# Kernel optimization log

Measured on AMD Instinct MI355X. Metric: run time of the kernel, lower is better.

## Reference

```python
import jax, jax.numpy as jnp
import numpy as np

P, N, C_IN, C_OUT = 40000, 32, 4, 64
C_AUG = C_IN + 5  # +3 cluster offsets, +2 center offsets -> 9
VX, VY = 0.2, 0.2
X_OFF = VX / 2 + 0.0      # 0.1
Y_OFF = VY / 2 + (-40.0)  # -39.9
BN_EPS = 1e-3


def setup_inputs() -> dict:
    key = jax.random.key(0)
    k1, k2, k3, k4, k5, k6, k7 = jax.random.split(key, 7)
    features = jax.random.normal(k1, (P, N, C_IN), dtype=jnp.float32)
    # at least 1 real point per pillar
    num_voxels = jax.random.randint(k2, (P,), 1, N + 1, dtype=jnp.int32)
    cx = jax.random.randint(k3, (P,), 0, 352, dtype=jnp.int32)  # x grid index (coors[:,3])
    cy = jax.random.randint(k4, (P,), 0, 400, dtype=jnp.int32)  # y grid index (coors[:,2])
    zeros = jnp.zeros((P,), dtype=jnp.int32)
    coors = jnp.stack([zeros, zeros, cy, cx], axis=1)  # [P,4] = (batch, z, y, x)
    linear_w = jax.random.normal(k5, (C_OUT, C_AUG), dtype=jnp.float32) * 0.1  # torch Linear weight [out,in], bias=False
    gamma = 1.0 + 0.1 * jax.random.normal(k6, (C_OUT,), dtype=jnp.float32)
    beta = 0.1 * jax.random.normal(k7, (C_OUT,), dtype=jnp.float32)
    return {
        "features": features,
        "num_voxels": num_voxels,
        "coors": coors,
        "linear_w": linear_w,
        "gamma": gamma,
        "beta": beta,
        "batch_size": 4,
    }


def reference(features, num_voxels, coors, linear_w, gamma, beta, batch_size):
    # batch_size=4 and P > 2500 -> lidar branch (self.linear / self.norm) of PFNLayer.
    dtype = features.dtype
    nv = num_voxels.astype(dtype)[:, None, None]  # [P,1,1]
    xyz = features[:, :, :3]
    points_mean = jnp.sum(xyz, axis=1, keepdims=True) / nv            # [P,1,3]
    f_cluster = xyz - points_mean                                     # [P,N,3]
    fcx = features[:, :, 0] - (coors[:, 3].astype(dtype)[:, None] * VX + X_OFF)
    fcy = features[:, :, 1] - (coors[:, 2].astype(dtype)[:, None] * VY + Y_OFF)
    f_center = jnp.stack([fcx, fcy], axis=-1)                         # [P,N,2]
    feats = jnp.concatenate([features, f_cluster, f_center], axis=-1)  # [P,N,9]
    # zero out padded points
    mask = (jnp.arange(N)[None, :] < num_voxels[:, None]).astype(dtype)[:, :, None]
    feats = feats * mask
    # Linear (no bias): [P,N,9] x [64,9]^T -> [P,N,64]
    x = jnp.einsum('pnc,uc->pnu', feats, linear_w)
    # BatchNorm1d in training mode: stats over (pillars, points) per channel, eps=1e-3
    mean = jnp.mean(x, axis=(0, 1))
    var = jnp.var(x, axis=(0, 1))
    x = (x - mean) * jax.lax.rsqrt(var + BN_EPS) * gamma + beta
    x = jax.nn.relu(x)
    # max over points, last_layer -> no concat; squeeze -> [P,64]
    return jnp.max(x, axis=1)
```

## Files before the change

kernel.cpp:

```cpp
#include <hip/hip_runtime.h>
#include <hip/hip_fp16.h>
#include <float.h>
#include <math.h>

#define PPIL   40000
#define NPTS   32
#define COUT   64
#define PPB    16
#define NBLK_F 2500
#define PSTRIDE 132
#define NSB_F  16
#define NFB    625

__device__ __forceinline__ float shfl_xor_f(float v, int m) {
    return __shfl_xor(v, m, 64);
}

__device__ __forceinline__ void weight_prep(const float* __restrict__ linear_w,
                                            float* lds_w, int tid)
{
    if (tid < 64) {
        const float* wr = linear_w + tid * 9;
        const float w0 = wr[0], w1 = wr[1], w2 = wr[2], w3 = wr[3], w4 = wr[4];
        const float w5 = wr[5], w6 = wr[6], w7 = wr[7], w8 = wr[8];
        float* dw = &lds_w[tid * 9];
        dw[0] = w0 + w4 + w7;
        dw[1] = w1 + w5 + w8;
        dw[2] = w2 + w6;
        dw[3] = w3;
        dw[4] = w4; dw[5] = w5; dw[6] = w6; dw[7] = w7; dw[8] = w8;
    }
}

__global__ __launch_bounds__(128) void pfn_main(
    const float* __restrict__ features, const int* __restrict__ num_voxels,
    const int* __restrict__ coors, const float* __restrict__ linear_w,
    __half* __restrict__ rawh, float* __restrict__ partials)
{
    __shared__ float lds_f[PPB * PSTRIDE];
    __shared__ float lds_w[64 * 9];

    const int tid = threadIdx.x;
    const int bid = blockIdx.x;
    const int pl2 = tid >> 3;
    const int cg  = tid & 7;
    const int p   = bid * PPB + pl2;

    weight_prep(linear_w, lds_w, tid);

    const int   nvi = num_voxels[p];
    const float nvf = (float)nvi;
    const float axp = (float)coors[p * 4 + 3] * 0.2f + 0.1f;
    const float byp = (float)coors[p * 4 + 2] * 0.2f - 39.9f;

    float sx = 0.f, sy = 0.f, sz = 0.f;
    float t0 = 0.f, t1 = 0.f, t2 = 0.f, t3 = 0.f;
    #pragma unroll
    for (int i = 0; i < 4; ++i) {
        const int n = cg + 8 * i;
        const float4 f = *(const float4*)(features + ((size_t)p * NPTS + n) * 4);
        *(float4*)&lds_f[pl2 * PSTRIDE + n * 4] = f;
        sx += f.x; sy += f.y; sz += f.z;
        const float m = (n < nvi) ? 1.0f : 0.0f;
        t0 = fmaf(f.x, m, t0); t1 = fmaf(f.y, m, t1);
        t2 = fmaf(f.z, m, t2); t3 = fmaf(f.w, m, t3);
    }
    #pragma unroll
    for (int m = 1; m <= 4; m <<= 1) {
        sx += shfl_xor_f(sx, m); sy += shfl_xor_f(sy, m); sz += shfl_xor_f(sz, m);
        t0 += shfl_xor_f(t0, m); t1 += shfl_xor_f(t1, m);
        t2 += shfl_xor_f(t2, m); t3 += shfl_xor_f(t3, m);
    }
    const float inv = 1.0f / nvf;
    const float mxp = sx * inv, myp = sy * inv, mzp = sz * inv;

    __syncthreads();

    float g0[8], g1[8], g2[8], g3[8], cc[8];
    #pragma unroll
    for (int k = 0; k < 8; ++k) {
        const float* wp = &lds_w[(cg * 8 + k) * 9];
        g0[k] = wp[0]; g1[k] = wp[1]; g2[k] = wp[2]; g3[k] = wp[3];
        cc[k] = -(wp[4] * mxp + wp[5] * myp + wp[6] * mzp + wp[7] * axp + wp[8] * byp);
    }

    float s2v[8], mxv[8];
    #pragma unroll
    for (int k = 0; k < 8; ++k) { s2v[k] = 0.0f; mxv[k] = -FLT_MAX; }

    const float4* fb = (const float4*)&lds_f[pl2 * PSTRIDE];
    for (int n = 0; n < nvi; ++n) {
        const float4 f = fb[n];
        #pragma unroll
        for (int k = 0; k < 8; ++k) {
            float x = fmaf(g0[k], f.x, cc[k]);
            x = fmaf(g1[k], f.y, x);
            x = fmaf(g2[k], f.z, x);
            x = fmaf(g3[k], f.w, x);
            s2v[k] = fmaf(x, x, s2v[k]);
            mxv[k] = fmaxf(mxv[k], x);
        }
    }
    if (nvi < NPTS) {
        #pragma unroll
        for (int k = 0; k < 8; ++k) mxv[k] = fmaxf(mxv[k], 0.0f);
    }

    float s1v[8];
    #pragma unroll
    for (int k = 0; k < 8; ++k) {
        float d = g0[k] * t0;
        d = fmaf(g1[k], t1, d);
        d = fmaf(g2[k], t2, d);
        d = fmaf(g3[k], t3, d);
        s1v[k] = fmaf(nvf, cc[k], d);
    }

    {
        __half2 h0 = __floats2half2_rn(mxv[0], mxv[1]);
        __half2 h1 = __floats2half2_rn(mxv[2], mxv[3]);
        __half2 h2 = __floats2half2_rn(mxv[4], mxv[5]);
        __half2 h3 = __floats2half2_rn(mxv[6], mxv[7]);
        uint4 pk;
        pk.x = *(const unsigned int*)&h0;
        pk.y = *(const unsigned int*)&h1;
        pk.z = *(const unsigned int*)&h2;
        pk.w = *(const unsigned int*)&h3;
        *(uint4*)(rawh + (size_t)p * COUT + cg * 8) = pk;
    }

    __syncthreads();
    float* lsum = lds_f;
    *(float4*)&lsum[pl2 * 128 + cg * 8 + 0]      = make_float4(s1v[0], s1v[1], s1v[2], s1v[3]);
    *(float4*)&lsum[pl2 * 128 + cg * 8 + 4]      = make_float4(s1v[4], s1v[5], s1v[6], s1v[7]);
    *(float4*)&lsum[pl2 * 128 + 64 + cg * 8 + 0] = make_float4(s2v[0], s2v[1], s2v[2], s2v[3]);
    *(float4*)&lsum[pl2 * 128 + 64 + cg * 8 + 4] = make_float4(s2v[4], s2v[5], s2v[6], s2v[7]);
    __syncthreads();

    float acc = 0.0f;
    #pragma unroll
    for (int r = 0; r < 16; ++r) acc += lsum[r * 128 + tid];
    partials[bid * 128 + tid] = acc;
}

__global__ __launch_bounds__(1024) void pfn_stats16(
    const float* __restrict__ partials, float* __restrict__ partials2)
{
    __shared__ double red[32][128];
    const int t = threadIdx.x, b = blockIdx.x;
    const int col4 = t & 31, j = t >> 5;
    const float4* p4 = (const float4*)partials;

    double a0 = 0.0, a1 = 0.0, a2 = 0.0, a3 = 0.0;
    #pragma unroll
    for (int i = 0; i < 5; ++i) {
        const int r = b + NSB_F * (j + 32 * i);
        if (r < NBLK_F) {
            const float4 v = p4[r * 32 + col4];
            a0 += (double)v.x; a1 += (double)v.y;
            a2 += (double)v.z; a3 += (double)v.w;
        }
    }
    red[j][col4 * 4 + 0] = a0;
    red[j][col4 * 4 + 1] = a1;
    red[j][col4 * 4 + 2] = a2;
    red[j][col4 * 4 + 3] = a3;
    __syncthreads();
    if (t < 128) {
        double s = 0.0;
        #pragma unroll
        for (int jj = 0; jj < 32; ++jj) s += red[jj][t];
        partials2[b * 128 + t] = (float)s;
    }
}

__global__ __launch_bounds__(1024) void pfn_final(
    const float* __restrict__ partials2, const float* __restrict__ gamma,
    const float* __restrict__ beta, const __half* __restrict__ rawh,
    float* __restrict__ out)
{
    __shared__ double red[128];
    __shared__ float  sb[128];
    const int t = threadIdx.x;
    if (t < 128) {
        double s = 0.0;
        #pragma unroll
        for (int b = 0; b < NSB_F; ++b) s += (double)partials2[b * 128 + t];
        red[t] = s;
    }
    __syncthreads();
    if (t < 64) {
        const float s1 = (float)red[t];
        const float s2 = (float)red[64 + t];
        const float invPN = 1.0f / ((float)PPIL * (float)NPTS);
        const float mean  = s1 * invPN;
        const float var   = fmaf(-mean, mean, s2 * invPN);
        const float scale = gamma[t] * rsqrtf(var + 1e-3f);
        sb[t]      = scale;
        sb[64 + t] = fmaf(-mean, scale, beta[t]);
    }
    __syncthreads();

    const int i  = blockIdx.x * 1024 + t;
    const int u0 = (i & 15) * 4;
    const uint2 pk = *(const uint2*)(rawh + (size_t)i * 4);
    const __half2 h01 = *(const __half2*)&pk.x;
    const __half2 h23 = *(const __half2*)&pk.y;
    float4 v;
    v.x = fmaxf(fmaf(__low2float(h01),  sb[u0 + 0], sb[64 + u0 + 0]), 0.0f);
    v.y = fmaxf(fmaf(__high2float(h01), sb[u0 + 1], sb[64 + u0 + 1]), 0.0f);
    v.z = fmaxf(fmaf(__low2float(h23),  sb[u0 + 2], sb[64 + u0 + 2]), 0.0f);
    v.w = fmaxf(fmaf(__high2float(h23), sb[u0 + 3], sb[64 + u0 + 3]), 0.0f);
    ((float4*)out)[i] = v;
}

extern "C" void kernel_launch(void* const* d_in, const int* in_sizes, int n_in,
                              void* d_out, int out_size, void* d_ws, size_t ws_size,
                              hipStream_t stream) {
    const float* features   = (const float*)d_in[0];
    const int*   num_voxels = (const int*)d_in[1];
    const int*   coors      = (const int*)d_in[2];
    const float* linear_w   = (const float*)d_in[3];
    const float* gamma      = (const float*)d_in[4];
    const float* beta       = (const float*)d_in[5];

    float*  out       = (float*)d_out;
    float*  wsf       = (float*)d_ws;
    float*  partials  = wsf;
    float*  partials2 = wsf + NBLK_F * 128;
    __half* rawh      = (__half*)(wsf + (1 << 20));

    pfn_main<<<NBLK_F, 128, 0, stream>>>(features, num_voxels, coors,
                                         linear_w, rawh, partials);
    pfn_stats16<<<NSB_F, 1024, 0, stream>>>(partials, partials2);
    pfn_final<<<NFB, 1024, 0, stream>>>(partials2, gamma, beta, rawh, out);
}
```

Baseline: 30.53 us.

## Process two pillar groups per block with register-prefetched second group

Each main-kernel block now handles 32 pillars in two sequential halves. The second half's features are loaded into registers while the first half computes. The weight-load and stats-reduction overhead is shared across both halves, and the partial-sum count and the stats kernel loop bounds are halved. The intent is to hide global-load latency and cut per-block fixed costs. The cost is fewer blocks (1250), higher register pressure from the prefetched float4s and the kept w4..w8 arrays, and possibly lower occupancy.

```diff
diff --git a/kernel.cpp b/kernel.cpp
--- a/kernel.cpp
+++ b/kernel.cpp
@@ -7,7 +7,7 @@
 #define NPTS   32
 #define COUT   64
 #define PPB    16
-#define NBLK_F 2500
+#define NBLK_M 1250
 #define PSTRIDE 132
 #define NSB_F  16
 #define NFB    625
@@ -32,6 +32,18 @@
     }
 }
 
+__device__ __forceinline__ void pillar_butterfly(
+    float& sx, float& sy, float& sz,
+    float& t0, float& t1, float& t2, float& t3)
+{
+    #pragma unroll
+    for (int m = 1; m <= 4; m <<= 1) {
+        sx += shfl_xor_f(sx, m); sy += shfl_xor_f(sy, m); sz += shfl_xor_f(sz, m);
+        t0 += shfl_xor_f(t0, m); t1 += shfl_xor_f(t1, m);
+        t2 += shfl_xor_f(t2, m); t3 += shfl_xor_f(t3, m);
+    }
+}
+
 __global__ __launch_bounds__(128) void pfn_main(
     const float* __restrict__ features, const int* __restrict__ num_voxels,
     const int* __restrict__ coors, const float* __restrict__ linear_w,
@@ -44,79 +56,85 @@
     const int bid = blockIdx.x;
     const int pl2 = tid >> 3;
     const int cg  = tid & 7;
-    const int p   = bid * PPB + pl2;
+    const int pA  = bid * (2 * PPB) + pl2;
+    const int pB  = bid * (2 * PPB) + PPB + pl2;
 
     weight_prep(linear_w, lds_w, tid);
 
-    const int   nvi = num_voxels[p];
-    const float nvf = (float)nvi;
-    const float axp = (float)coors[p * 4 + 3] * 0.2f + 0.1f;
-    const float byp = (float)coors[p * 4 + 2] * 0.2f - 39.9f;
-
-    float sx = 0.f, sy = 0.f, sz = 0.f;
-    float t0 = 0.f, t1 = 0.f, t2 = 0.f, t3 = 0.f;
+    const int   nviA = num_voxels[pA];
+    const float nvfA = (float)nviA;
+    const float axA  = (float)coors[pA * 4 + 3] * 0.2f + 0.1f;
+    const float byA  = (float)coors[pA * 4 + 2] * 0.2f - 39.9f;
+
+    float sxA = 0.f, syA = 0.f, szA = 0.f;
+    float tA0 = 0.f, tA1 = 0.f, tA2 = 0.f, tA3 = 0.f;
     #pragma unroll
     for (int i = 0; i < 4; ++i) {
         const int n = cg + 8 * i;
-        const float4 f = *(const float4*)(features + ((size_t)p * NPTS + n) * 4);
+        const float4 f = *(const float4*)(features + ((size_t)pA * NPTS + n) * 4);
         *(float4*)&lds_f[pl2 * PSTRIDE + n * 4] = f;
-        sx += f.x; sy += f.y; sz += f.z;
-        const float m = (n < nvi) ? 1.0f : 0.0f;
-        t0 = fmaf(f.x, m, t0); t1 = fmaf(f.y, m, t1);
-        t2 = fmaf(f.z, m, t2); t3 = fmaf(f.w, m, t3);
-    }
-    #pragma unroll
-    for (int m = 1; m <= 4; m <<= 1) {
-        sx += shfl_xor_f(sx, m); sy += shfl_xor_f(sy, m); sz += shfl_xor_f(sz, m);
-        t0 += shfl_xor_f(t0, m); t1 += shfl_xor_f(t1, m);
-        t2 += shfl_xor_f(t2, m); t3 += shfl_xor_f(t3, m);
-    }
-    const float inv = 1.0f / nvf;
-    const float mxp = sx * inv, myp = sy * inv, mzp = sz * inv;
-
-    __syncthreads();
-
-    float g0[8], g1[8], g2[8], g3[8], cc[8];
+        sxA += f.x; syA += f.y; szA += f.z;
+        const float m = (n < nviA) ? 1.0f : 0.0f;
+        tA0 = fmaf(f.x, m, tA0); tA1 = fmaf(f.y, m, tA1);
+        tA2 = fmaf(f.z, m, tA2); tA3 = fmaf(f.w, m, tA3);
+    }
+    pillar_butterfly(sxA, syA, szA, tA0, tA1, tA2, tA3);
+    const float invA = 1.0f / nvfA;
+    const float mxpA = sxA * invA, mypA = syA * invA, mzpA = szA * invA;
+
+    __syncthreads();
+
+    const int   nviB = num_voxels[pB];
+    const float nvfB = (float)nviB;
+    const float axB  = (float)coors[pB * 4 + 3] * 0.2f + 0.1f;
+    const float byB  = (float)coors[pB * 4 + 2] * 0.2f - 39.9f;
+    float4 fB[4];
+    #pragma unroll
+    for (int i = 0; i < 4; ++i) {
+        const int n = cg + 8 * i;
+        fB[i] = *(const float4*)(features + ((size_t)pB * NPTS + n) * 4);
+    }
+
+    float g0[8], g1[8], g2[8], g3[8], w4[8], w5[8], w6[8], w7[8], w8[8];
+    float cc[8];
     #pragma unroll
     for (int k = 0; k < 8; ++k) {
         const float* wp = &lds_w[(cg * 8 + k) * 9];
         g0[k] = wp[0]; g1[k] = wp[1]; g2[k] = wp[2]; g3[k] = wp[3];
-        cc[k] = -(wp[4] * mxp + wp[5] * myp + wp[6] * mzp + wp[7] * axp + wp[8] * byp);
-    }
-
-    float s2v[8], mxv[8];
-    #pragma unroll
-    for (int k = 0; k < 8; ++k) { s2v[k] = 0.0f; mxv[k] = -FLT_MAX; }
-
-    const float4* fb = (const float4*)&lds_f[pl2 * PSTRIDE];
-    for (int n = 0; n < nvi; ++n) {
-        const float4 f = fb[n];
+        w4[k] = wp[4]; w5[k] = wp[5]; w6[k] = wp[6]; w7[k] = wp[7]; w8[k] = wp[8];
+        cc[k] = -(w4[k] * mxpA + w5[k] * mypA + w6[k] * mzpA + w7[k] * axA + w8[k] * byA);
+    }
+
+    float s1acc[8], s2acc[8], mxv[8];
+
+    #pragma unroll
+    for (int k = 0; k < 8; ++k) { s2acc[k] = 0.0f; mxv[k] = -FLT_MAX; }
+    {
+        const float4* fb = (const float4*)&lds_f[pl2 * PSTRIDE];
+        for (int n = 0; n < nviA; ++n) {
+            const float4 f = fb[n];
+            #pragma unroll
+            for (int k = 0; k < 8; ++k) {
+                float x = fmaf(g0[k], f.x, cc[k]);
+                x = fmaf(g1[k], f.y, x);
+                x = fmaf(g2[k], f.z, x);
+                x = fmaf(g3[k], f.w, x);
+                s2acc[k] = fmaf(x, x, s2acc[k]);
+                mxv[k]   = fmaxf(mxv[k], x);
+            }
+        }
+        if (nviA < NPTS) {
+            #pragma unroll
+            for (int k = 0; k < 8; ++k) mxv[k] = fmaxf(mxv[k], 0.0f);
+        }
         #pragma unroll
         for (int k = 0; k < 8; ++k) {
-            float x = fmaf(g0[k], f.x, cc[k]);
-            x = fmaf(g1[k], f.y, x);
-            x = fmaf(g2[k], f.z, x);
-            x = fmaf(g3[k], f.w, x);
-            s2v[k] = fmaf(x, x, s2v[k]);
-            mxv[k] = fmaxf(mxv[k], x);
-        }
-    }
-    if (nvi < NPTS) {
-        #pragma unroll
-        for (int k = 0; k < 8; ++k) mxv[k] = fmaxf(mxv[k], 0.0f);
-    }
-
-    float s1v[8];
-    #pragma unroll
-    for (int k = 0; k < 8; ++k) {
-        float d = g0[k] * t0;
-        d = fmaf(g1[k], t1, d);
-        d = fmaf(g2[k], t2, d);
-        d = fmaf(g3[k], t3, d);
-        s1v[k] = fmaf(nvf, cc[k], d);
-    }
-
-    {
+            float d = g0[k] * tA0;
+            d = fmaf(g1[k], tA1, d);
+            d = fmaf(g2[k], tA2, d);
+            d = fmaf(g3[k], tA3, d);
+            s1acc[k] = fmaf(nvfA, cc[k], d);
+        }
         __half2 h0 = __floats2half2_rn(mxv[0], mxv[1]);
         __half2 h1 = __floats2half2_rn(mxv[2], mxv[3]);
         __half2 h2 = __floats2half2_rn(mxv[4], mxv[5]);
@@ -126,15 +144,78 @@
         pk.y = *(const unsigned int*)&h1;
         pk.z = *(const unsigned int*)&h2;
         pk.w = *(const unsigned int*)&h3;
-        *(uint4*)(rawh + (size_t)p * COUT + cg * 8) = pk;
+        *(uint4*)(rawh + (size_t)pA * COUT + cg * 8) = pk;
+    }
+
+    __syncthreads();
+
+    float sxB = 0.f, syB = 0.f, szB = 0.f;
+    float tB0 = 0.f, tB1 = 0.f, tB2 = 0.f, tB3 = 0.f;
+    #pragma unroll
+    for (int i = 0; i < 4; ++i) {
+        const int n = cg + 8 * i;
+        *(float4*)&lds_f[pl2 * PSTRIDE + n * 4] = fB[i];
+        sxB += fB[i].x; syB += fB[i].y; szB += fB[i].z;
+        const float m = (n < nviB) ? 1.0f : 0.0f;
+        tB0 = fmaf(fB[i].x, m, tB0); tB1 = fmaf(fB[i].y, m, tB1);
+        tB2 = fmaf(fB[i].z, m, tB2); tB3 = fmaf(fB[i].w, m, tB3);
+    }
+    pillar_butterfly(sxB, syB, szB, tB0, tB1, tB2, tB3);
+    const float invB = 1.0f / nvfB;
+    const float mxpB = sxB * invB, mypB = syB * invB, mzpB = szB * invB;
+    #pragma unroll
+    for (int k = 0; k < 8; ++k)
+        cc[k] = -(w4[k] * mxpB + w5[k] * mypB + w6[k] * mzpB + w7[k] * axB + w8[k] * byB);
+    __syncthreads();
+
+    {
+        float s2v[8];
+        #pragma unroll
+        for (int k = 0; k < 8; ++k) { s2v[k] = 0.0f; mxv[k] = -FLT_MAX; }
+        const float4* fb = (const float4*)&lds_f[pl2 * PSTRIDE];
+        for (int n = 0; n < nviB; ++n) {
+            const float4 f = fb[n];
+            #pragma unroll
+            for (int k = 0; k < 8; ++k) {
+                float x = fmaf(g0[k], f.x, cc[k]);
+                x = fmaf(g1[k], f.y, x);
+                x = fmaf(g2[k], f.z, x);
+                x = fmaf(g3[k], f.w, x);
+                s2v[k] = fmaf(x, x, s2v[k]);
+                mxv[k] = fmaxf(mxv[k], x);
+            }
+        }
+        if (nviB < NPTS) {
+            #pragma unroll
+            for (int k = 0; k < 8; ++k) mxv[k] = fmaxf(mxv[k], 0.0f);
+        }
+        #pragma unroll
+        for (int k = 0; k < 8; ++k) {
+            float d = g0[k] * tB0;
+            d = fmaf(g1[k], tB1, d);
+            d = fmaf(g2[k], tB2, d);
+            d = fmaf(g3[k], tB3, d);
+            s1acc[k] += fmaf(nvfB, cc[k], d);
+            s2acc[k] += s2v[k];
+        }
+        __half2 h0 = __floats2half2_rn(mxv[0], mxv[1]);
+        __half2 h1 = __floats2half2_rn(mxv[2], mxv[3]);
+        __half2 h2 = __floats2half2_rn(mxv[4], mxv[5]);
+        __half2 h3 = __floats2half2_rn(mxv[6], mxv[7]);
+        uint4 pk;
+        pk.x = *(const unsigned int*)&h0;
+        pk.y = *(const unsigned int*)&h1;
+        pk.z = *(const unsigned int*)&h2;
+        pk.w = *(const unsigned int*)&h3;
+        *(uint4*)(rawh + (size_t)pB * COUT + cg * 8) = pk;
     }
 
     __syncthreads();
     float* lsum = lds_f;
-    *(float4*)&lsum[pl2 * 128 + cg * 8 + 0]      = make_float4(s1v[0], s1v[1], s1v[2], s1v[3]);
-    *(float4*)&lsum[pl2 * 128 + cg * 8 + 4]      = make_float4(s1v[4], s1v[5], s1v[6], s1v[7]);
-    *(float4*)&lsum[pl2 * 128 + 64 + cg * 8 + 0] = make_float4(s2v[0], s2v[1], s2v[2], s2v[3]);
-    *(float4*)&lsum[pl2 * 128 + 64 + cg * 8 + 4] = make_float4(s2v[4], s2v[5], s2v[6], s2v[7]);
+    *(float4*)&lsum[pl2 * 128 + cg * 8 + 0]      = make_float4(s1acc[0], s1acc[1], s1acc[2], s1acc[3]);
+    *(float4*)&lsum[pl2 * 128 + cg * 8 + 4]      = make_float4(s1acc[4], s1acc[5], s1acc[6], s1acc[7]);
+    *(float4*)&lsum[pl2 * 128 + 64 + cg * 8 + 0] = make_float4(s2acc[0], s2acc[1], s2acc[2], s2acc[3]);
+    *(float4*)&lsum[pl2 * 128 + 64 + cg * 8 + 4] = make_float4(s2acc[4], s2acc[5], s2acc[6], s2acc[7]);
     __syncthreads();
 
     float acc = 0.0f;
@@ -153,9 +234,9 @@
 
     double a0 = 0.0, a1 = 0.0, a2 = 0.0, a3 = 0.0;
     #pragma unroll
-    for (int i = 0; i < 5; ++i) {
+    for (int i = 0; i < 3; ++i) {
         const int r = b + NSB_F * (j + 32 * i);
-        if (r < NBLK_F) {
+        if (r < NBLK_M) {
             const float4 v = p4[r * 32 + col4];
             a0 += (double)v.x; a1 += (double)v.y;
             a2 += (double)v.z; a3 += (double)v.w;
@@ -227,10 +308,10 @@
     float*  out       = (float*)d_out;
     float*  wsf       = (float*)d_ws;
     float*  partials  = wsf;
-    float*  partials2 = wsf + NBLK_F * 128;
+    float*  partials2 = wsf + NBLK_M * 128;
     __half* rawh      = (__half*)(wsf + (1 << 20));
 
-    pfn_main<<<NBLK_F, 128, 0, stream>>>(features, num_voxels, coors,
+    pfn_main<<<NBLK_M, 128, 0, stream>>>(features, num_voxels, coors,
                                          linear_w, rawh, partials);
     pfn_stats16<<<NSB_F, 1024, 0, stream>>>(partials, partials2);
     pfn_final<<<NFB, 1024, 0, stream>>>(partials2, gamma, beta, rawh, out);
```

After: 31.90 us. 4.5% more time.

## Remap main kernel so each lane owns one output channel across pillars

Applied to the files above, without the earlier changes.

The main kernel now uses 256-thread blocks covering 32 pillars. Instead of 8 threads per pillar each handling 8 channels, each wave lane owns one channel and loops over 8 pillars, reading per-pillar constants staged in LDS. The point loop is unrolled by two. This is meant to cut register pressure and block count and to balance work across variable nv, at the cost of 2-byte scattered half stores instead of 16-byte packed stores and a serial loop over pillars per wave.

```diff
diff --git a/kernel.cpp b/kernel.cpp
--- a/kernel.cpp
+++ b/kernel.cpp
@@ -6,8 +6,8 @@
 #define PPIL   40000
 #define NPTS   32
 #define COUT   64
-#define PPB    16
-#define NBLK_F 2500
+#define PPB    32
+#define NBLK_M 1250
 #define PSTRIDE 132
 #define NSB_F  16
 #define NFB    625
@@ -16,9 +16,20 @@
     return __shfl_xor(v, m, 64);
 }
 
-__device__ __forceinline__ void weight_prep(const float* __restrict__ linear_w,
-                                            float* lds_w, int tid)
+__global__ __launch_bounds__(256) void pfn_main(
+    const float* __restrict__ features, const int* __restrict__ num_voxels,
+    const int* __restrict__ coors, const float* __restrict__ linear_w,
+    __half* __restrict__ rawh, float* __restrict__ partials)
 {
+    __shared__ float lds_f[PPB * PSTRIDE];
+    __shared__ float lds_pc[PPB][12];
+    __shared__ float lds_w[64 * 9];
+    __shared__ float lds_red[4][128];
+
+    const int tid = threadIdx.x;
+    const int bid = blockIdx.x;
+    const int pb  = bid * PPB;
+
     if (tid < 64) {
         const float* wr = linear_w + tid * 9;
         const float w0 = wr[0], w1 = wr[1], w2 = wr[2], w3 = wr[3], w4 = wr[4];
@@ -30,117 +41,111 @@
         dw[3] = w3;
         dw[4] = w4; dw[5] = w5; dw[6] = w6; dw[7] = w7; dw[8] = w8;
     }
-}
-
-__global__ __launch_bounds__(128) void pfn_main(
-    const float* __restrict__ features, const int* __restrict__ num_voxels,
-    const int* __restrict__ coors, const float* __restrict__ linear_w,
-    __half* __restrict__ rawh, float* __restrict__ partials)
-{
-    __shared__ float lds_f[PPB * PSTRIDE];
-    __shared__ float lds_w[64 * 9];
-
-    const int tid = threadIdx.x;
-    const int bid = blockIdx.x;
-    const int pl2 = tid >> 3;
-    const int cg  = tid & 7;
-    const int p   = bid * PPB + pl2;
-
-    weight_prep(linear_w, lds_w, tid);
-
-    const int   nvi = num_voxels[p];
-    const float nvf = (float)nvi;
-    const float axp = (float)coors[p * 4 + 3] * 0.2f + 0.1f;
-    const float byp = (float)coors[p * 4 + 2] * 0.2f - 39.9f;
-
-    float sx = 0.f, sy = 0.f, sz = 0.f;
-    float t0 = 0.f, t1 = 0.f, t2 = 0.f, t3 = 0.f;
+
+    {
+        const int pl  = tid >> 3, sub = tid & 7;
+        const int p   = pb + pl;
+        const int nvi = num_voxels[p];
+        float sx = 0.f, sy = 0.f, sz = 0.f;
+        float t0 = 0.f, t1 = 0.f, t2 = 0.f, t3 = 0.f;
+        #pragma unroll
+        for (int i = 0; i < 4; ++i) {
+            const int n = sub + 8 * i;
+            const float4 f = *(const float4*)(features + ((size_t)p * NPTS + n) * 4);
+            *(float4*)&lds_f[pl * PSTRIDE + n * 4] = f;
+            sx += f.x; sy += f.y; sz += f.z;
+            const float m = (n < nvi) ? 1.0f : 0.0f;
+            t0 = fmaf(f.x, m, t0); t1 = fmaf(f.y, m, t1);
+            t2 = fmaf(f.z, m, t2); t3 = fmaf(f.w, m, t3);
+        }
+        #pragma unroll
+        for (int m = 1; m <= 4; m <<= 1) {
+            sx += shfl_xor_f(sx, m); sy += shfl_xor_f(sy, m); sz += shfl_xor_f(sz, m);
+            t0 += shfl_xor_f(t0, m); t1 += shfl_xor_f(t1, m);
+            t2 += shfl_xor_f(t2, m); t3 += shfl_xor_f(t3, m);
+        }
+        if (sub == 0) {
+            const float nvf = (float)nvi;
+            const float inv = 1.0f / nvf;
+            float* pc = lds_pc[pl];
+            pc[0] = sx * inv;
+            pc[1] = sy * inv;
+            pc[2] = sz * inv;
+            pc[3] = (float)coors[p * 4 + 3] * 0.2f + 0.1f;
+            pc[4] = (float)coors[p * 4 + 2] * 0.2f - 39.9f;
+            pc[5] = nvf;
+            pc[6] = t0; pc[7] = t1; pc[8] = t2; pc[9] = t3;
+        }
+    }
+    __syncthreads();
+
+    const int w    = tid >> 6;
+    const int lane = tid & 63;
+
+    const float* wp = &lds_w[lane * 9];
+    const float g0 = wp[0], g1 = wp[1], g2 = wp[2], g3 = wp[3];
+    const float w4 = wp[4], w5 = wp[5], w6 = wp[6], w7 = wp[7], w8 = wp[8];
+
+    float s1acc = 0.0f, s2acc = 0.0f;
+
     #pragma unroll
-    for (int i = 0; i < 4; ++i) {
-        const int n = cg + 8 * i;
-        const float4 f = *(const float4*)(features + ((size_t)p * NPTS + n) * 4);
-        *(float4*)&lds_f[pl2 * PSTRIDE + n * 4] = f;
-        sx += f.x; sy += f.y; sz += f.z;
-        const float m = (n < nvi) ? 1.0f : 0.0f;
-        t0 = fmaf(f.x, m, t0); t1 = fmaf(f.y, m, t1);
-        t2 = fmaf(f.z, m, t2); t3 = fmaf(f.w, m, t3);
-    }
-    #pragma unroll
-    for (int m = 1; m <= 4; m <<= 1) {
-        sx += shfl_xor_f(sx, m); sy += shfl_xor_f(sy, m); sz += shfl_xor_f(sz, m);
-        t0 += shfl_xor_f(t0, m); t1 += shfl_xor_f(t1, m);
-        t2 += shfl_xor_f(t2, m); t3 += shfl_xor_f(t3, m);
-    }
-    const float inv = 1.0f / nvf;
-    const float mxp = sx * inv, myp = sy * inv, mzp = sz * inv;
-
-    __syncthreads();
-
-    float g0[8], g1[8], g2[8], g3[8], cc[8];
-    #pragma unroll
-    for (int k = 0; k < 8; ++k) {
-        const float* wp = &lds_w[(cg * 8 + k) * 9];
-        g0[k] = wp[0]; g1[k] = wp[1]; g2[k] = wp[2]; g3[k] = wp[3];
-        cc[k] = -(wp[4] * mxp + wp[5] * myp + wp[6] * mzp + wp[7] * axp + wp[8] * byp);
-    }
-
-    float s2v[8], mxv[8];
-    #pragma unroll
-    for (int k = 0; k < 8; ++k) { s2v[k] = 0.0f; mxv[k] = -FLT_MAX; }
-
-    const float4* fb = (const float4*)&lds_f[pl2 * PSTRIDE];
-    for (int n = 0; n < nvi; ++n) {
-        const float4 f = fb[n];
-        #pragma unroll
-        for (int k = 0; k < 8; ++k) {
-            float x = fmaf(g0[k], f.x, cc[k]);
-            x = fmaf(g1[k], f.y, x);
-            x = fmaf(g2[k], f.z, x);
-            x = fmaf(g3[k], f.w, x);
-            s2v[k] = fmaf(x, x, s2v[k]);
-            mxv[k] = fmaxf(mxv[k], x);
-        }
-    }
-    if (nvi < NPTS) {
-        #pragma unroll
-        for (int k = 0; k < 8; ++k) mxv[k] = fmaxf(mxv[k], 0.0f);
-    }
-
-    float s1v[8];
-    #pragma unroll
-    for (int k = 0; k < 8; ++k) {
-        float d = g0[k] * t0;
-        d = fmaf(g1[k], t1, d);
-        d = fmaf(g2[k], t2, d);
-        d = fmaf(g3[k], t3, d);
-        s1v[k] = fmaf(nvf, cc[k], d);
-    }
-
-    {
-        __half2 h0 = __floats2half2_rn(mxv[0], mxv[1]);
-        __half2 h1 = __floats2half2_rn(mxv[2], mxv[3]);
-        __half2 h2 = __floats2half2_rn(mxv[4], mxv[5]);
-        __half2 h3 = __floats2half2_rn(mxv[6], mxv[7]);
-        uint4 pk;
-        pk.x = *(const unsigned int*)&h0;
-        pk.y = *(const unsigned int*)&h1;
-        pk.z = *(const unsigned int*)&h2;
-        pk.w = *(const unsigned int*)&h3;
-        *(uint4*)(rawh + (size_t)p * COUT + cg * 8) = pk;
-    }
-
-    __syncthreads();
-    float* lsum = lds_f;
-    *(float4*)&lsum[pl2 * 128 + cg * 8 + 0]      = make_float4(s1v[0], s1v[1], s1v[2], s1v[3]);
-    *(float4*)&lsum[pl2 * 128 + cg * 8 + 4]      = make_float4(s1v[4], s1v[5], s1v[6], s1v[7]);
-    *(float4*)&lsum[pl2 * 128 + 64 + cg * 8 + 0] = make_float4(s2v[0], s2v[1], s2v[2], s2v[3]);
-    *(float4*)&lsum[pl2 * 128 + 64 + cg * 8 + 4] = make_float4(s2v[4], s2v[5], s2v[6], s2v[7]);
-    __syncthreads();
-
-    float acc = 0.0f;
-    #pragma unroll
-    for (int r = 0; r < 16; ++r) acc += lsum[r * 128 + tid];
-    partials[bid * 128 + tid] = acc;
+    for (int i = 0; i < 8; ++i) {
+        const int pl = w * 8 + i;
+        const float* pc = lds_pc[pl];
+        const float mxp = pc[0], myp = pc[1], mzp = pc[2];
+        const float axp = pc[3], byp = pc[4], nvf = pc[5];
+        const float Fm0 = pc[6], Fm1 = pc[7], Fm2 = pc[8], Fm3 = pc[9];
+        const int   nvi = (int)nvf;
+
+        float cc = -(w4 * mxp + w5 * myp + w6 * mzp + w7 * axp + w8 * byp);
+
+        float s2 = 0.0f, mx = -FLT_MAX;
+        const float4* fb = (const float4*)&lds_f[pl * PSTRIDE];
+        int n = 0;
+        for (; n + 2 <= nvi; n += 2) {
+            const float4 fa = fb[n];
+            const float4 fc = fb[n + 1];
+            float xa = fmaf(g0, fa.x, cc);
+            xa = fmaf(g1, fa.y, xa);
+            xa = fmaf(g2, fa.z, xa);
+            xa = fmaf(g3, fa.w, xa);
+            float xb = fmaf(g0, fc.x, cc);
+            xb = fmaf(g1, fc.y, xb);
+            xb = fmaf(g2, fc.z, xb);
+            xb = fmaf(g3, fc.w, xb);
+            s2 = fmaf(xa, xa, s2);
+            s2 = fmaf(xb, xb, s2);
+            mx = fmaxf(mx, fmaxf(xa, xb));
+        }
+        if (n < nvi) {
+            const float4 fa = fb[n];
+            float xa = fmaf(g0, fa.x, cc);
+            xa = fmaf(g1, fa.y, xa);
+            xa = fmaf(g2, fa.z, xa);
+            xa = fmaf(g3, fa.w, xa);
+            s2 = fmaf(xa, xa, s2);
+            mx = fmaxf(mx, xa);
+        }
+        if (nvi < NPTS) mx = fmaxf(mx, 0.0f);
+
+        float d = g0 * Fm0;
+        d = fmaf(g1, Fm1, d);
+        d = fmaf(g2, Fm2, d);
+        d = fmaf(g3, Fm3, d);
+        s1acc += fmaf(nvf, cc, d);
+        s2acc += s2;
+
+        rawh[(size_t)(pb + pl) * COUT + lane] = __float2half(mx);
+    }
+
+    lds_red[w][lane]      = s1acc;
+    lds_red[w][64 + lane] = s2acc;
+    __syncthreads();
+    if (tid < 128) {
+        const float acc = lds_red[0][tid] + lds_red[1][tid] +
+                          lds_red[2][tid] + lds_red[3][tid];
+        partials[bid * 128 + tid] = acc;
+    }
 }
 
 __global__ __launch_bounds__(1024) void pfn_stats16(
@@ -153,9 +158,9 @@
 
     double a0 = 0.0, a1 = 0.0, a2 = 0.0, a3 = 0.0;
     #pragma unroll
-    for (int i = 0; i < 5; ++i) {
+    for (int i = 0; i < 3; ++i) {
         const int r = b + NSB_F * (j + 32 * i);
-        if (r < NBLK_F) {
+        if (r < NBLK_M) {
             const float4 v = p4[r * 32 + col4];
             a0 += (double)v.x; a1 += (double)v.y;
             a2 += (double)v.z; a3 += (double)v.w;
@@ -227,10 +232,10 @@
     float*  out       = (float*)d_out;
     float*  wsf       = (float*)d_ws;
     float*  partials  = wsf;
-    float*  partials2 = wsf + NBLK_F * 128;
+    float*  partials2 = wsf + NBLK_M * 128;
     __half* rawh      = (__half*)(wsf + (1 << 20));
 
-    pfn_main<<<NBLK_F, 128, 0, stream>>>(features, num_voxels, coors,
+    pfn_main<<<NBLK_M, 256, 0, stream>>>(features, num_voxels, coors,
                                          linear_w, rawh, partials);
     pfn_stats16<<<NSB_F, 1024, 0, stream>>>(partials, partials2);
     pfn_final<<<NFB, 1024, 0, stream>>>(partials2, gamma, beta, rawh, out);
```

Result: faster. 28.65 us (median of 4 runs) (-6.1%).
